# Kernel tuning notes

Hardware: AMD Instinct MI355X
Metric: run time of the kernel (lower is better)

Reference implementation:

```python
import jax, jax.numpy as jnp
import numpy as np

EPS = 1e-5


def _bn(x):
    # BatchNorm2d in training mode with gamma=1, beta=0 (as initialized in the module)
    m = x.mean(axis=(0, 2, 3), keepdims=True)
    v = jnp.mean((x - m) ** 2, axis=(0, 2, 3), keepdims=True)
    return (x - m) * jax.lax.rsqrt(v + EPS)


def _adder2d(x, w, stride, padding):
    # AdderNet pseudo-conv: out = -sum_{cin,kh,kw} |patch - w|  (negative L1 distance)
    Cout, Cin, k, _ = w.shape
    p = jax.lax.conv_general_dilated_patches(
        x, (k, k), (stride, stride), [(padding, padding), (padding, padding)]
    )  # [B, Cin*k*k, Ho, Wo], channel-major patch order matching torch unfold
    B, CKK, Ho, Wo = p.shape
    pf = p.reshape(B, CKK, Ho * Wo)          # [B, CKK, L]
    wf = w.reshape(Cout, CKK)                # [Cout, CKK]
    out = -jnp.abs(pf[:, None, :, :] - wf[None, :, :, None]).sum(axis=2)  # [B, Cout, L]
    return out.reshape(B, Cout, Ho, Wo)


def _block(x, w1, w2, stride=1, down_w=None):
    out = jax.nn.relu(_bn(_adder2d(x, w1, stride, 1)))
    out = _bn(_adder2d(out, w2, 1, 1))
    if down_w is None:
        identity = x
    else:
        identity = _bn(_adder2d(x, down_w, stride, 0))
    return jax.nn.relu(out + identity)


def setup_inputs() -> dict:
    key = jax.random.key(0)
    ks = jax.random.split(key, 10)
    f = lambda k, s: jax.random.normal(k, s, dtype=jnp.float32)
    return {
        "x": f(ks[0], (32, 3, 32, 32)),
        "conv1_w": f(ks[1], (16, 3, 3, 3)) * 0.2,
        "l1_w": f(ks[2], (6, 16, 16, 3, 3)) * 0.2,
        "l2_w0": f(ks[3], (32, 16, 3, 3)) * 0.2,
        "l2_ws": f(ks[4], (5, 32, 32, 3, 3)) * 0.2,
        "l2_down": f(ks[5], (32, 16, 1, 1)) * 0.2,
        "l3_w0": f(ks[6], (64, 32, 3, 3)) * 0.2,
        "l3_ws": f(ks[7], (5, 64, 64, 3, 3)) * 0.2,
        "l3_down": f(ks[8], (64, 32, 1, 1)) * 0.2,
        "fc_w": f(ks[9], (10, 64, 1, 1)) * 0.2,
    }


def reference(x, conv1_w, l1_w, l2_w0, l2_ws, l2_down, l3_w0, l3_ws, l3_down, fc_w):
    h = jax.lax.conv(x, conv1_w, (1, 1), 'SAME')  # ordinary conv stem
    h = jax.nn.relu(_bn(h))
    # layer1: 3 blocks, 16 channels, stride 1, no downsample
    for i in range(3):
        h = _block(h, l1_w[2 * i], l1_w[2 * i + 1], 1, None)
    # layer2: first block stride 2 with 1x1 adder downsample
    h = _block(h, l2_w0, l2_ws[0], 2, l2_down)
    h = _block(h, l2_ws[1], l2_ws[2], 1, None)
    h = _block(h, l2_ws[3], l2_ws[4], 1, None)
    # layer3
    h = _block(h, l3_w0, l3_ws[0], 2, l3_down)
    h = _block(h, l3_ws[1], l3_ws[2], 1, None)
    h = _block(h, l3_ws[3], l3_ws[4], 1, None)
    # AvgPool2d(8) on an 8x8 map == global mean
    h = h.mean(axis=(2, 3), keepdims=True)  # [B, 64, 1, 1]
    h = jnp.einsum('bchw,oc->bohw', h, fc_w[:, :, 0, 0])  # 1x1 conv classifier
    h = _bn(h)
    return h.reshape(h.shape[0], -1)  # [B, num_classes]
```

## Files before the change

### kernel.cpp

```cpp
#include <hip/hip_runtime.h>

#define BN_EPS 1e-5f

template<int C>
__device__ __forceinline__ void stats_prologue(const float2* __restrict__ part,
                                               int nPart, float invN,
                                               float2* smr, float2* pred) {
  const int TPC = 256 / C;
  int c  = threadIdx.x / TPC;
  int sl = threadIdx.x - c * TPC;
  float s = 0.f, s2 = 0.f;
  for (int j = sl; j < nPart; j += TPC) {
    float2 p = part[c * nPart + j];
    s += p.x; s2 += p.y;
  }
  pred[threadIdx.x] = make_float2(s, s2);
  __syncthreads();
  for (int st = TPC >> 1; st; st >>= 1) {
    if (sl < st) {
      pred[threadIdx.x].x += pred[threadIdx.x + st].x;
      pred[threadIdx.x].y += pred[threadIdx.x + st].y;
    }
    __syncthreads();
  }
  if (sl == 0) {
    float m   = pred[threadIdx.x].x * invN;
    float var = fmaxf(pred[threadIdx.x].y * invN - m * m, 0.f);
    smr[c] = make_float2(m, rsqrtf(var + BN_EPS));
  }
  __syncthreads();
}

template<int K, int CT, int CIN, bool INBN>
__global__ void __launch_bounds__(256)
adder_k(const float* __restrict__ x, const float2* __restrict__ inpart,
        int nPartIn, float invNIn,
        const float* __restrict__ w,
        float* __restrict__ raw, float2* __restrict__ partials,
        int B, int Cout, int H, int W, int Ho, int Wo, int stride, int pad) {
  __shared__ float2 smr[INBN ? CIN : 1];
  __shared__ float2 pred[256];
  if (INBN) stats_prologue<CIN>(inpart, nPartIn, invNIn, smr, pred);

  const int KK  = K * K;
  const int HWo = Ho * Wo;
  const int i   = blockIdx.x * 256 + threadIdx.x;
  const int b   = i / HWo;
  const int hw  = i - b * HWo;
  const int ho  = hw / Wo, wo = hw - ho * Wo;
  const int co0 = blockIdx.y * CT;

  int  off[K * K];
  bool valid[K * K];
  #pragma unroll
  for (int kh = 0; kh < K; kh++) {
    int hh = ho * stride + kh - pad;
    bool hv = (hh >= 0) & (hh < H);
    #pragma unroll
    for (int kw = 0; kw < K; kw++) {
      int ww = wo * stride + kw - pad;
      valid[kh * K + kw] = hv & (ww >= 0) & (ww < W);
      off[kh * K + kw]   = hh * W + ww;
    }
  }

  float acc[CT];
  #pragma unroll
  for (int c = 0; c < CT; c++) acc[c] = 0.f;

  const float* xb = x + (b * CIN) * H * W;
  for (int cb = 0; cb < CIN; cb += 4) {
    float p[4][K * K];
    #pragma unroll
    for (int u = 0; u < 4; u++) {
      const float* xp = xb + (cb + u) * H * W;
      float m = 0.f, r = 0.f;
      if (INBN) { float2 t = smr[cb + u]; m = t.x; r = t.y; }
      #pragma unroll
      for (int t = 0; t < KK; t++) {
        float v = valid[t] ? xp[off[t]] : 0.f;
        if (INBN) v = valid[t] ? fmaxf((v - m) * r, 0.f) : 0.f;
        p[u][t] = v;
      }
    }
    #pragma unroll
    for (int c = 0; c < CT; c++) {
      const float* wp = w + ((co0 + c) * CIN + cb) * KK;
      #pragma unroll
      for (int u = 0; u < 4; u++)
        #pragma unroll
        for (int t = 0; t < KK; t++)
          acc[c] += fabsf(p[u][t] - wp[u * KK + t]);
    }
  }

  __shared__ float2 bred[4][CT];
  float2 mine[CT];
  #pragma unroll
  for (int c = 0; c < CT; c++) {
    float v = -acc[c];
    raw[(b * Cout + co0 + c) * HWo + hw] = v;
    float sx = v, sy = v * v;
    #pragma unroll
    for (int o2 = 32; o2; o2 >>= 1) {
      sx += __shfl_down(sx, o2, 64);
      sy += __shfl_down(sy, o2, 64);
    }
    mine[c] = make_float2(sx, sy);
  }
  int lane = threadIdx.x & 63, wid = threadIdx.x >> 6;
  if (lane == 0) {
    #pragma unroll
    for (int c = 0; c < CT; c++) bred[wid][c] = mine[c];
  }
  __syncthreads();
  if (threadIdx.x < CT) {
    float2 t = bred[0][threadIdx.x];
    #pragma unroll
    for (int wv = 1; wv < 4; wv++) { t.x += bred[wv][threadIdx.x].x; t.y += bred[wv][threadIdx.x].y; }
    partials[(co0 + threadIdx.x) * gridDim.x + blockIdx.x] = t;
  }
}

__global__ void __launch_bounds__(256)
conv_stem_bn(const float* __restrict__ x, const float* __restrict__ w,
             float* __restrict__ raw, float2* __restrict__ partials) {
  const int co = blockIdx.y;
  const int i = blockIdx.x * 256 + threadIdx.x;
  const int b = i >> 10, hw = i & 1023;
  const int ho = hw >> 5, wo = hw & 31;
  float acc = 0.f;
  #pragma unroll
  for (int ci = 0; ci < 3; ci++) {
    const float* xp = x + (b * 3 + ci) * 1024;
    #pragma unroll
    for (int kh = 0; kh < 3; kh++) {
      int hh = ho + kh - 1;
      bool hv = (hh >= 0) & (hh < 32);
      #pragma unroll
      for (int kw = 0; kw < 3; kw++) {
        int ww = wo + kw - 1;
        float xv = (hv & (ww >= 0) & (ww < 32)) ? xp[hh * 32 + ww] : 0.f;
        acc += xv * w[((co * 3 + ci) * 3 + kh) * 3 + kw];
      }
    }
  }
  raw[(b * 16 + co) * 1024 + hw] = acc;

  float sx = acc, sy = acc * acc;
  #pragma unroll
  for (int o2 = 32; o2; o2 >>= 1) {
    sx += __shfl_down(sx, o2, 64);
    sy += __shfl_down(sy, o2, 64);
  }
  __shared__ float2 red[4];
  int lane = threadIdx.x & 63, wid = threadIdx.x >> 6;
  if (lane == 0) red[wid] = make_float2(sx, sy);
  __syncthreads();
  if (threadIdx.x == 0) {
    float2 t = red[0];
    t.x += red[1].x + red[2].x + red[3].x;
    t.y += red[1].y + red[2].y + red[3].y;
    partials[co * 128 + blockIdx.x] = t;
  }
}

template<int IDMODE, int C, bool POOL>
__global__ void __launch_bounds__(256)
combine_k(const float* __restrict__ raw2, const float2* __restrict__ part2, int nPart2,
          const float* __restrict__ idsrc, const float2* __restrict__ partI, int nPartI,
          float invN, float* __restrict__ out, int HW) {
  __shared__ float2 s2[C];
  __shared__ float2 sI[IDMODE ? C : 1];
  __shared__ float2 pred[256];
  stats_prologue<C>(part2, nPart2, invN, s2, pred);
  if (IDMODE) stats_prologue<C>(partI, nPartI, invN, sI, pred);

  int idx = blockIdx.x * 256 + threadIdx.x;
  int c = (idx / HW) % C;
  float2 t2 = s2[c];
  float y = (raw2[idx] - t2.x) * t2.y;
  float id;
  if (IDMODE == 0) id = idsrc[idx];
  else {
    float2 tI = sI[c];
    id = (idsrc[idx] - tI.x) * tI.y;
    if (IDMODE == 2) id = fmaxf(id, 0.f);
  }
  float h = fmaxf(y + id, 0.f);
  if (!POOL) {
    out[idx] = h;
  } else {
    float s = h;
    #pragma unroll
    for (int o2 = 32; o2; o2 >>= 1) s += __shfl_down(s, o2, 64);
    if ((threadIdx.x & 63) == 0) out[idx >> 6] = s * (1.f / 64.f);
  }
}

__global__ void head_k(const float* __restrict__ pooled, const float* __restrict__ fcw,
                       float* __restrict__ out) {
  __shared__ float logits[320];
  __shared__ float mn[10], rs[10];
  int t = threadIdx.x;
  if (t < 320) {
    int b = t / 10, o = t - b * 10;
    float s = 0.f;
    #pragma unroll
    for (int c = 0; c < 64; c++) s += pooled[b * 64 + c] * fcw[o * 64 + c];
    logits[t] = s;
  }
  __syncthreads();
  if (t < 10) {
    float s = 0.f;
    for (int b = 0; b < 32; b++) s += logits[b * 10 + t];
    float m = s * (1.f / 32.f);
    float v = 0.f;
    for (int b = 0; b < 32; b++) { float d = logits[b * 10 + t] - m; v += d * d; }
    mn[t] = m;
    rs[t] = rsqrtf(v * (1.f / 32.f) + BN_EPS);
  }
  __syncthreads();
  if (t < 320) out[t] = (logits[t] - mn[t % 10]) * rs[t % 10];
}

extern "C" void kernel_launch(void* const* d_in, const int* in_sizes, int n_in,
                              void* d_out, int out_size, void* d_ws, size_t ws_size,
                              hipStream_t stream) {
  const float* x      = (const float*)d_in[0];
  const float* conv1w = (const float*)d_in[1];
  const float* l1w    = (const float*)d_in[2];
  const float* l2w0   = (const float*)d_in[3];
  const float* l2ws   = (const float*)d_in[4];
  const float* l2down = (const float*)d_in[5];
  const float* l3w0   = (const float*)d_in[6];
  const float* l3ws   = (const float*)d_in[7];
  const float* l3down = (const float*)d_in[8];
  const float* fcw    = (const float*)d_in[9];
  float* out = (float*)d_out;

  const int T2MB = 32 * 16 * 32 * 32;
  float* base = (float*)d_ws;
  float* R0 = base + 0 * T2MB;
  float* RA = base + 1 * T2MB;
  float* RB = base + 2 * T2MB;
  float* RD = base + 3 * T2MB;
  float* H0 = base + 4 * T2MB;
  float* H1 = base + 5 * T2MB;
  float* pooled = base + 6 * T2MB;
  float2* partS = (float2*)(pooled + 4096);
  float2* partA = partS + 4096;
  float2* partB = partA + 4096;
  float2* partD = partB + 4096;

  const float inv1 = 1.f / 32768.f;
  const float inv2 = 1.f / 8192.f;
  const float inv3 = 1.f / 2048.f;

  conv_stem_bn<<<dim3(128, 16), 256, 0, stream>>>(x, conv1w, R0, partS);

  float* cur = H1;
  float* nxt = H0;

  {
    const dim3 ag(128, 8);
    adder_k<3, 2, 16, true ><<<ag, 256, 0, stream>>>(R0, partS, 128, inv1, l1w + 0 * 2304, RA, partA, 32, 16, 32, 32, 32, 32, 1, 1);
    adder_k<3, 2, 16, true ><<<ag, 256, 0, stream>>>(RA, partA, 128, inv1, l1w + 1 * 2304, RB, partB, 32, 16, 32, 32, 32, 32, 1, 1);
    combine_k<2, 16, false><<<2048, 256, 0, stream>>>(RB, partB, 128, R0, partS, 128, inv1, nxt, 1024);
    { float* t = cur; cur = nxt; nxt = t; }
    for (int i = 1; i < 3; i++) {
      adder_k<3, 2, 16, false><<<ag, 256, 0, stream>>>(cur, nullptr, 0, 0.f, l1w + (2 * i) * 2304, RA, partA, 32, 16, 32, 32, 32, 32, 1, 1);
      adder_k<3, 2, 16, true ><<<ag, 256, 0, stream>>>(RA, partA, 128, inv1, l1w + (2 * i + 1) * 2304, RB, partB, 32, 16, 32, 32, 32, 32, 1, 1);
      combine_k<0, 16, false><<<2048, 256, 0, stream>>>(RB, partB, 128, cur, nullptr, 0, inv1, nxt, 1024);
      float* t = cur; cur = nxt; nxt = t;
    }
  }

  {
    const dim3 ag(32, 16);
    adder_k<3, 2, 16, false><<<ag, 256, 0, stream>>>(cur, nullptr, 0, 0.f, l2w0, RA, partA, 32, 32, 32, 32, 16, 16, 2, 1);
    adder_k<3, 2, 32, true ><<<ag, 256, 0, stream>>>(RA, partA, 32, inv2, l2ws + 0 * 9216, RB, partB, 32, 32, 16, 16, 16, 16, 1, 1);
    adder_k<1, 2, 16, false><<<ag, 256, 0, stream>>>(cur, nullptr, 0, 0.f, l2down, RD, partD, 32, 32, 32, 32, 16, 16, 2, 0);
    combine_k<1, 32, false><<<1024, 256, 0, stream>>>(RB, partB, 32, RD, partD, 32, inv2, nxt, 256);
    { float* t = cur; cur = nxt; nxt = t; }
    for (int i = 0; i < 2; i++) {
      adder_k<3, 2, 32, false><<<ag, 256, 0, stream>>>(cur, nullptr, 0, 0.f, l2ws + (1 + 2 * i) * 9216, RA, partA, 32, 32, 16, 16, 16, 16, 1, 1);
      adder_k<3, 2, 32, true ><<<ag, 256, 0, stream>>>(RA, partA, 32, inv2, l2ws + (2 + 2 * i) * 9216, RB, partB, 32, 32, 16, 16, 16, 16, 1, 1);
      combine_k<0, 32, false><<<1024, 256, 0, stream>>>(RB, partB, 32, cur, nullptr, 0, inv2, nxt, 256);
      float* t = cur; cur = nxt; nxt = t;
    }
  }

  {
    const dim3 ag(8, 64);
    adder_k<3, 1, 32, false><<<ag, 256, 0, stream>>>(cur, nullptr, 0, 0.f, l3w0, RA, partA, 32, 64, 16, 16, 8, 8, 2, 1);
    adder_k<3, 1, 64, true ><<<ag, 256, 0, stream>>>(RA, partA, 8, inv3, l3ws + 0 * 36864, RB, partB, 32, 64, 8, 8, 8, 8, 1, 1);
    adder_k<1, 1, 32, false><<<ag, 256, 0, stream>>>(cur, nullptr, 0, 0.f, l3down, RD, partD, 32, 64, 16, 16, 8, 8, 2, 0);
    combine_k<1, 64, false><<<512, 256, 0, stream>>>(RB, partB, 8, RD, partD, 8, inv3, nxt, 64);
    { float* t = cur; cur = nxt; nxt = t; }
    adder_k<3, 1, 64, false><<<ag, 256, 0, stream>>>(cur, nullptr, 0, 0.f, l3ws + 1 * 36864, RA, partA, 32, 64, 8, 8, 8, 8, 1, 1);
    adder_k<3, 1, 64, true ><<<ag, 256, 0, stream>>>(RA, partA, 8, inv3, l3ws + 2 * 36864, RB, partB, 32, 64, 8, 8, 8, 8, 1, 1);
    combine_k<0, 64, false><<<512, 256, 0, stream>>>(RB, partB, 8, cur, nullptr, 0, inv3, nxt, 64);
    { float* t = cur; cur = nxt; nxt = t; }
    adder_k<3, 1, 64, false><<<ag, 256, 0, stream>>>(cur, nullptr, 0, 0.f, l3ws + 3 * 36864, RA, partA, 32, 64, 8, 8, 8, 8, 1, 1);
    adder_k<3, 1, 64, true ><<<ag, 256, 0, stream>>>(RA, partA, 8, inv3, l3ws + 4 * 36864, RB, partB, 32, 64, 8, 8, 8, 8, 1, 1);
    combine_k<0, 64, true ><<<512, 256, 0, stream>>>(RB, partB, 8, cur, nullptr, 0, inv3, pooled, 64);
  }

  head_k<<<1, 320, 0, stream>>>(pooled, fcw, out);
}
```

Before: 406.3 us.

## Split adder convolutions over input-channel chunks with separate reduction kernels

Replaces the per-output-channel-tile adder kernel with a split-K version: each block handles 4 output channels and 8 input channels, writing partial L1 sums to scratch planes, and a new reduce kernel sums the planes, writes raw outputs and produces BN partial statistics. The 1x1 downsample branch is fused into the strided 3x3 kernel by reusing the center tap. The goal is more parallelism and shorter per-thread loops in the small late layers, at the cost of extra kernel launches and extra global traffic for the partial planes.

```diff
diff --git a/kernel.cpp b/kernel.cpp
--- a/kernel.cpp
+++ b/kernel.cpp
@@ -31,94 +31,151 @@
   __syncthreads();
 }
 
-template<int K, int CT, int CIN, bool INBN>
-__global__ void __launch_bounds__(256)
-adder_k(const float* __restrict__ x, const float2* __restrict__ inpart,
-        int nPartIn, float invNIn,
-        const float* __restrict__ w,
-        float* __restrict__ raw, float2* __restrict__ partials,
-        int B, int Cout, int H, int W, int Ho, int Wo, int stride, int pad) {
+template<int CIN, bool INBN, bool DOWN>
+__global__ void __launch_bounds__(256, 4)
+adder_s1(const float* __restrict__ x, const float2* __restrict__ inpart,
+         int nPartIn, float invNIn,
+         const float* __restrict__ w, const float* __restrict__ wD,
+         float* __restrict__ pout, float* __restrict__ poutD,
+         int B, int Cout, int H, int W, int Ho, int Wo,
+         int stride, int pad, int plane) {
   __shared__ float2 smr[INBN ? CIN : 1];
-  __shared__ float2 pred[256];
+  __shared__ float2 pred[INBN ? 256 : 1];
   if (INBN) stats_prologue<CIN>(inpart, nPartIn, invNIn, smr, pred);
 
-  const int KK  = K * K;
   const int HWo = Ho * Wo;
   const int i   = blockIdx.x * 256 + threadIdx.x;
   const int b   = i / HWo;
   const int hw  = i - b * HWo;
   const int ho  = hw / Wo, wo = hw - ho * Wo;
-  const int co0 = blockIdx.y * CT;
-
-  int  off[K * K];
-  bool valid[K * K];
-  #pragma unroll
-  for (int kh = 0; kh < K; kh++) {
+  const int co0 = blockIdx.y * 4;
+  const int ci0 = blockIdx.z * 8;
+
+  int  off[9];
+  bool valid[9];
+  #pragma unroll
+  for (int kh = 0; kh < 3; kh++) {
     int hh = ho * stride + kh - pad;
     bool hv = (hh >= 0) & (hh < H);
     #pragma unroll
-    for (int kw = 0; kw < K; kw++) {
+    for (int kw = 0; kw < 3; kw++) {
       int ww = wo * stride + kw - pad;
-      valid[kh * K + kw] = hv & (ww >= 0) & (ww < W);
-      off[kh * K + kw]   = hh * W + ww;
-    }
-  }
-
-  float acc[CT];
-  #pragma unroll
-  for (int c = 0; c < CT; c++) acc[c] = 0.f;
-
-  const float* xb = x + (b * CIN) * H * W;
-  for (int cb = 0; cb < CIN; cb += 4) {
-    float p[4][K * K];
-    #pragma unroll
-    for (int u = 0; u < 4; u++) {
-      const float* xp = xb + (cb + u) * H * W;
-      float m = 0.f, r = 0.f;
-      if (INBN) { float2 t = smr[cb + u]; m = t.x; r = t.y; }
+      valid[kh * 3 + kw] = hv & (ww >= 0) & (ww < W);
+      off[kh * 3 + kw]   = hh * W + ww;
+    }
+  }
+
+  float p[8][9];
+  #pragma unroll
+  for (int u = 0; u < 8; u++) {
+    const float* xp = x + (b * CIN + ci0 + u) * H * W;
+    float m = 0.f, r = 0.f;
+    if (INBN) { float2 t = smr[ci0 + u]; m = t.x; r = t.y; }
+    #pragma unroll
+    for (int t = 0; t < 9; t++) {
+      float v = valid[t] ? xp[off[t]] : 0.f;
+      if (INBN) v = valid[t] ? fmaxf((v - m) * r, 0.f) : 0.f;
+      p[u][t] = v;
+    }
+  }
+
+  float acc[4];
+  float accD[DOWN ? 4 : 1];
+  #pragma unroll
+  for (int c = 0; c < 4; c++) acc[c] = 0.f;
+  if (DOWN) {
+    #pragma unroll
+    for (int c = 0; c < 4; c++) accD[c] = 0.f;
+  }
+
+  #pragma unroll
+  for (int c = 0; c < 4; c++) {
+    const float* wp = w + ((co0 + c) * CIN + ci0) * 9;
+    #pragma unroll
+    for (int u = 0; u < 8; u++)
       #pragma unroll
-      for (int t = 0; t < KK; t++) {
-        float v = valid[t] ? xp[off[t]] : 0.f;
-        if (INBN) v = valid[t] ? fmaxf((v - m) * r, 0.f) : 0.f;
-        p[u][t] = v;
-      }
-    }
-    #pragma unroll
-    for (int c = 0; c < CT; c++) {
-      const float* wp = w + ((co0 + c) * CIN + cb) * KK;
+      for (int t = 0; t < 9; t++)
+        acc[c] += fabsf(p[u][t] - wp[u * 9 + t]);
+    if (DOWN) {
+      const float* wdp = wD + (co0 + c) * CIN + ci0;
       #pragma unroll
-      for (int u = 0; u < 4; u++)
-        #pragma unroll
-        for (int t = 0; t < KK; t++)
-          acc[c] += fabsf(p[u][t] - wp[u * KK + t]);
-    }
-  }
-
-  __shared__ float2 bred[4][CT];
-  float2 mine[CT];
-  #pragma unroll
-  for (int c = 0; c < CT; c++) {
-    float v = -acc[c];
-    raw[(b * Cout + co0 + c) * HWo + hw] = v;
+      for (int u = 0; u < 8; u++)
+        accD[c] += fabsf(p[u][4] - wdp[u]);
+    }
+  }
+
+  const int zb = blockIdx.z * plane;
+  #pragma unroll
+  for (int c = 0; c < 4; c++) {
+    pout[zb + (b * Cout + co0 + c) * HWo + hw] = acc[c];
+    if (DOWN) poutD[zb + (b * Cout + co0 + c) * HWo + hw] = accD[c];
+  }
+}
+
+template<int NC, bool DUAL, bool BR>
+__global__ void __launch_bounds__(256)
+reduce_k(const float* __restrict__ pin, float* __restrict__ raw, float2* __restrict__ parts,
+         const float* __restrict__ pinD, float* __restrict__ rawD, float2* __restrict__ partsD,
+         int Cout, int HWo, int plane, int nPart) {
+  const int e = blockIdx.x * 256 + threadIdx.x;
+  const int b  = e / (Cout * HWo);
+  const int r  = e - b * Cout * HWo;
+  const int co = r / HWo;
+  const int hw = r - co * HWo;
+  const int lane = threadIdx.x & 63, wid = threadIdx.x >> 6;
+  __shared__ float2 bb[4];
+
+  {
+    float s = 0.f;
+    #pragma unroll
+    for (int z = 0; z < NC; z++) s += pin[z * plane + e];
+    float v = -s;
+    raw[e] = v;
     float sx = v, sy = v * v;
     #pragma unroll
     for (int o2 = 32; o2; o2 >>= 1) {
       sx += __shfl_down(sx, o2, 64);
       sy += __shfl_down(sy, o2, 64);
     }
-    mine[c] = make_float2(sx, sy);
-  }
-  int lane = threadIdx.x & 63, wid = threadIdx.x >> 6;
-  if (lane == 0) {
-    #pragma unroll
-    for (int c = 0; c < CT; c++) bred[wid][c] = mine[c];
-  }
-  __syncthreads();
-  if (threadIdx.x < CT) {
-    float2 t = bred[0][threadIdx.x];
-    #pragma unroll
-    for (int wv = 1; wv < 4; wv++) { t.x += bred[wv][threadIdx.x].x; t.y += bred[wv][threadIdx.x].y; }
-    partials[(co0 + threadIdx.x) * gridDim.x + blockIdx.x] = t;
+    if (BR) {
+      if (lane == 0) bb[wid] = make_float2(sx, sy);
+      __syncthreads();
+      if (threadIdx.x == 0) {
+        float2 t = bb[0];
+        t.x += bb[1].x + bb[2].x + bb[3].x;
+        t.y += bb[1].y + bb[2].y + bb[3].y;
+        parts[co * nPart + ((b * HWo + hw) >> 8)] = t;
+      }
+    } else {
+      if (lane == 0) parts[co * nPart + ((b * HWo + hw) >> 6)] = make_float2(sx, sy);
+    }
+  }
+
+  if (DUAL) {
+    if (BR) __syncthreads();
+    float s = 0.f;
+    #pragma unroll
+    for (int z = 0; z < NC; z++) s += pinD[z * plane + e];
+    float v = -s;
+    rawD[e] = v;
+    float sx = v, sy = v * v;
+    #pragma unroll
+    for (int o2 = 32; o2; o2 >>= 1) {
+      sx += __shfl_down(sx, o2, 64);
+      sy += __shfl_down(sy, o2, 64);
+    }
+    if (BR) {
+      if (lane == 0) bb[wid] = make_float2(sx, sy);
+      __syncthreads();
+      if (threadIdx.x == 0) {
+        float2 t = bb[0];
+        t.x += bb[1].x + bb[2].x + bb[3].x;
+        t.y += bb[1].y + bb[2].y + bb[3].y;
+        partsD[co * nPart + ((b * HWo + hw) >> 8)] = t;
+      }
+    } else {
+      if (lane == 0) partsD[co * nPart + ((b * HWo + hw) >> 6)] = make_float2(sx, sy);
+    }
   }
 }
 
@@ -247,64 +304,84 @@
   float* RD = base + 3 * T2MB;
   float* H0 = base + 4 * T2MB;
   float* H1 = base + 5 * T2MB;
-  float* pooled = base + 6 * T2MB;
-  float2* partS = (float2*)(pooled + 4096);
+  float* PA = base + 6 * T2MB;
+  float* PD = base + 8 * T2MB;
+  float* sm = base + 9 * T2MB;
+  float* pooled = sm;
+  float2* partS = (float2*)(sm + 4096);
   float2* partA = partS + 4096;
   float2* partB = partA + 4096;
   float2* partD = partB + 4096;
 
+  const int B = 32;
   const float inv1 = 1.f / 32768.f;
   const float inv2 = 1.f / 8192.f;
   const float inv3 = 1.f / 2048.f;
 
+  const int pl1 = 32 * 16 * 1024;
+  const int pl2 = 32 * 32 * 256;
+  const int pl3 = 32 * 64 * 64;
+
   conv_stem_bn<<<dim3(128, 16), 256, 0, stream>>>(x, conv1w, R0, partS);
 
   float* cur = H1;
   float* nxt = H0;
 
   {
-    const dim3 ag(128, 8);
-    adder_k<3, 2, 16, true ><<<ag, 256, 0, stream>>>(R0, partS, 128, inv1, l1w + 0 * 2304, RA, partA, 32, 16, 32, 32, 32, 32, 1, 1);
-    adder_k<3, 2, 16, true ><<<ag, 256, 0, stream>>>(RA, partA, 128, inv1, l1w + 1 * 2304, RB, partB, 32, 16, 32, 32, 32, 32, 1, 1);
-    combine_k<2, 16, false><<<2048, 256, 0, stream>>>(RB, partB, 128, R0, partS, 128, inv1, nxt, 1024);
-    { float* t = cur; cur = nxt; nxt = t; }
-    for (int i = 1; i < 3; i++) {
-      adder_k<3, 2, 16, false><<<ag, 256, 0, stream>>>(cur, nullptr, 0, 0.f, l1w + (2 * i) * 2304, RA, partA, 32, 16, 32, 32, 32, 32, 1, 1);
-      adder_k<3, 2, 16, true ><<<ag, 256, 0, stream>>>(RA, partA, 128, inv1, l1w + (2 * i + 1) * 2304, RB, partB, 32, 16, 32, 32, 32, 32, 1, 1);
-      combine_k<0, 16, false><<<2048, 256, 0, stream>>>(RB, partB, 128, cur, nullptr, 0, inv1, nxt, 1024);
+    const dim3 ag(128, 4, 2);
+    for (int i = 0; i < 3; i++) {
+      const float* w1 = l1w + (2 * i) * 2304;
+      const float* w2 = l1w + (2 * i + 1) * 2304;
+      if (i == 0)
+        adder_s1<16, true , false><<<ag, 256, 0, stream>>>(R0, partS, 128, inv1, w1, nullptr, PA, nullptr, B, 16, 32, 32, 32, 32, 1, 1, pl1);
+      else
+        adder_s1<16, false, false><<<ag, 256, 0, stream>>>(cur, nullptr, 0, 0.f, w1, nullptr, PA, nullptr, B, 16, 32, 32, 32, 32, 1, 1, pl1);
+      reduce_k<2, false, true><<<2048, 256, 0, stream>>>(PA, RA, partA, nullptr, nullptr, nullptr, 16, 1024, pl1, 128);
+      adder_s1<16, true , false><<<ag, 256, 0, stream>>>(RA, partA, 128, inv1, w2, nullptr, PA, nullptr, B, 16, 32, 32, 32, 32, 1, 1, pl1);
+      reduce_k<2, false, true><<<2048, 256, 0, stream>>>(PA, RB, partB, nullptr, nullptr, nullptr, 16, 1024, pl1, 128);
+      if (i == 0)
+        combine_k<2, 16, false><<<2048, 256, 0, stream>>>(RB, partB, 128, R0, partS, 128, inv1, nxt, 1024);
+      else
+        combine_k<0, 16, false><<<2048, 256, 0, stream>>>(RB, partB, 128, cur, nullptr, 0, inv1, nxt, 1024);
       float* t = cur; cur = nxt; nxt = t;
     }
   }
 
   {
-    const dim3 ag(32, 16);
-    adder_k<3, 2, 16, false><<<ag, 256, 0, stream>>>(cur, nullptr, 0, 0.f, l2w0, RA, partA, 32, 32, 32, 32, 16, 16, 2, 1);
-    adder_k<3, 2, 32, true ><<<ag, 256, 0, stream>>>(RA, partA, 32, inv2, l2ws + 0 * 9216, RB, partB, 32, 32, 16, 16, 16, 16, 1, 1);
-    adder_k<1, 2, 16, false><<<ag, 256, 0, stream>>>(cur, nullptr, 0, 0.f, l2down, RD, partD, 32, 32, 32, 32, 16, 16, 2, 0);
+    adder_s1<16, false, true ><<<dim3(32, 8, 2), 256, 0, stream>>>(cur, nullptr, 0, 0.f, l2w0, l2down, PA, PD, B, 32, 32, 32, 16, 16, 2, 1, pl2);
+    reduce_k<2, true , true><<<1024, 256, 0, stream>>>(PA, RA, partA, PD, RD, partD, 32, 256, pl2, 32);
+    adder_s1<32, true , false><<<dim3(32, 8, 4), 256, 0, stream>>>(RA, partA, 32, inv2, l2ws + 0 * 9216, nullptr, PA, nullptr, B, 32, 16, 16, 16, 16, 1, 1, pl2);
+    reduce_k<4, false, true><<<1024, 256, 0, stream>>>(PA, RB, partB, nullptr, nullptr, nullptr, 32, 256, pl2, 32);
     combine_k<1, 32, false><<<1024, 256, 0, stream>>>(RB, partB, 32, RD, partD, 32, inv2, nxt, 256);
     { float* t = cur; cur = nxt; nxt = t; }
     for (int i = 0; i < 2; i++) {
-      adder_k<3, 2, 32, false><<<ag, 256, 0, stream>>>(cur, nullptr, 0, 0.f, l2ws + (1 + 2 * i) * 9216, RA, partA, 32, 32, 16, 16, 16, 16, 1, 1);
-      adder_k<3, 2, 32, true ><<<ag, 256, 0, stream>>>(RA, partA, 32, inv2, l2ws + (2 + 2 * i) * 9216, RB, partB, 32, 32, 16, 16, 16, 16, 1, 1);
+      adder_s1<32, false, false><<<dim3(32, 8, 4), 256, 0, stream>>>(cur, nullptr, 0, 0.f, l2ws + (1 + 2 * i) * 9216, nullptr, PA, nullptr, B, 32, 16, 16, 16, 16, 1, 1, pl2);
+      reduce_k<4, false, true><<<1024, 256, 0, stream>>>(PA, RA, partA, nullptr, nullptr, nullptr, 32, 256, pl2, 32);
+      adder_s1<32, true , false><<<dim3(32, 8, 4), 256, 0, stream>>>(RA, partA, 32, inv2, l2ws + (2 + 2 * i) * 9216, nullptr, PA, nullptr, B, 32, 16, 16, 16, 16, 1, 1, pl2);
+      reduce_k<4, false, true><<<1024, 256, 0, stream>>>(PA, RB, partB, nullptr, nullptr, nullptr, 32, 256, pl2, 32);
       combine_k<0, 32, false><<<1024, 256, 0, stream>>>(RB, partB, 32, cur, nullptr, 0, inv2, nxt, 256);
       float* t = cur; cur = nxt; nxt = t;
     }
   }
 
   {
-    const dim3 ag(8, 64);
-    adder_k<3, 1, 32, false><<<ag, 256, 0, stream>>>(cur, nullptr, 0, 0.f, l3w0, RA, partA, 32, 64, 16, 16, 8, 8, 2, 1);
-    adder_k<3, 1, 64, true ><<<ag, 256, 0, stream>>>(RA, partA, 8, inv3, l3ws + 0 * 36864, RB, partB, 32, 64, 8, 8, 8, 8, 1, 1);
-    adder_k<1, 1, 32, false><<<ag, 256, 0, stream>>>(cur, nullptr, 0, 0.f, l3down, RD, partD, 32, 64, 16, 16, 8, 8, 2, 0);
-    combine_k<1, 64, false><<<512, 256, 0, stream>>>(RB, partB, 8, RD, partD, 8, inv3, nxt, 64);
+    adder_s1<32, false, true ><<<dim3(8, 16, 4), 256, 0, stream>>>(cur, nullptr, 0, 0.f, l3w0, l3down, PA, PD, B, 64, 16, 16, 8, 8, 2, 1, pl3);
+    reduce_k<4, true , false><<<512, 256, 0, stream>>>(PA, RA, partA, PD, RD, partD, 64, 64, pl3, 32);
+    adder_s1<64, true , false><<<dim3(8, 16, 8), 256, 0, stream>>>(RA, partA, 32, inv3, l3ws + 0 * 36864, nullptr, PA, nullptr, B, 64, 8, 8, 8, 8, 1, 1, pl3);
+    reduce_k<8, false, false><<<512, 256, 0, stream>>>(PA, RB, partB, nullptr, nullptr, nullptr, 64, 64, pl3, 32);
+    combine_k<1, 64, false><<<512, 256, 0, stream>>>(RB, partB, 32, RD, partD, 32, inv3, nxt, 64);
     { float* t = cur; cur = nxt; nxt = t; }
-    adder_k<3, 1, 64, false><<<ag, 256, 0, stream>>>(cur, nullptr, 0, 0.f, l3ws + 1 * 36864, RA, partA, 32, 64, 8, 8, 8, 8, 1, 1);
-    adder_k<3, 1, 64, true ><<<ag, 256, 0, stream>>>(RA, partA, 8, inv3, l3ws + 2 * 36864, RB, partB, 32, 64, 8, 8, 8, 8, 1, 1);
-    combine_k<0, 64, false><<<512, 256, 0, stream>>>(RB, partB, 8, cur, nullptr, 0, inv3, nxt, 64);
-    { float* t = cur; cur = nxt; nxt = t; }
-    adder_k<3, 1, 64, false><<<ag, 256, 0, stream>>>(cur, nullptr, 0, 0.f, l3ws + 3 * 36864, RA, partA, 32, 64, 8, 8, 8, 8, 1, 1);
-    adder_k<3, 1, 64, true ><<<ag, 256, 0, stream>>>(RA, partA, 8, inv3, l3ws + 4 * 36864, RB, partB, 32, 64, 8, 8, 8, 8, 1, 1);
-    combine_k<0, 64, true ><<<512, 256, 0, stream>>>(RB, partB, 8, cur, nullptr, 0, inv3, pooled, 64);
+    for (int i = 0; i < 2; i++) {
+      adder_s1<64, false, false><<<dim3(8, 16, 8), 256, 0, stream>>>(cur, nullptr, 0, 0.f, l3ws + (1 + 2 * i) * 36864, nullptr, PA, nullptr, B, 64, 8, 8, 8, 8, 1, 1, pl3);
+      reduce_k<8, false, false><<<512, 256, 0, stream>>>(PA, RA, partA, nullptr, nullptr, nullptr, 64, 64, pl3, 32);
+      adder_s1<64, true , false><<<dim3(8, 16, 8), 256, 0, stream>>>(RA, partA, 32, inv3, l3ws + (2 + 2 * i) * 36864, nullptr, PA, nullptr, B, 64, 8, 8, 8, 8, 1, 1, pl3);
+      reduce_k<8, false, false><<<512, 256, 0, stream>>>(PA, RB, partB, nullptr, nullptr, nullptr, 64, 64, pl3, 32);
+      if (i == 1)
+        combine_k<0, 64, true ><<<512, 256, 0, stream>>>(RB, partB, 32, cur, nullptr, 0, inv3, pooled, 64);
+      else
+        combine_k<0, 64, false><<<512, 256, 0, stream>>>(RB, partB, 32, cur, nullptr, 0, inv3, nxt, 64);
+      if (i == 0) { float* t = cur; cur = nxt; nxt = t; }
+    }
   }
 
   head_k<<<1, 320, 0, stream>>>(pooled, fcw, out);
```

Result: faster. 370.1 us (-8.9%).

## Fuse residual combine and downsample into adder kernels, split Cin across waves

Applied to the files above, without the earlier changes.

Drops the separate combine kernels by applying the previous block's BN, residual add and ReLU on the fly while loading the next adder's inputs, writing the hidden activation out as a side effect. The 1x1 downsample adder is computed inside the strided 3x3 adder using the centre tap. Each block now splits input channels across its four waves with 64 positions per block and reduces through shared memory, which gives more blocks and more parallelism. The cost is extra residual reads per input tap, plus shared-memory reduction and more template variants.

```diff
diff --git a/kernel.cpp b/kernel.cpp
--- a/kernel.cpp
+++ b/kernel.cpp
@@ -26,99 +26,130 @@
   if (sl == 0) {
     float m   = pred[threadIdx.x].x * invN;
     float var = fmaxf(pred[threadIdx.x].y * invN - m * m, 0.f);
-    smr[c] = make_float2(m, rsqrtf(var + BN_EPS));
-  }
-  __syncthreads();
-}
-
-template<int K, int CT, int CIN, bool INBN>
-__global__ void __launch_bounds__(256)
-adder_k(const float* __restrict__ x, const float2* __restrict__ inpart,
-        int nPartIn, float invNIn,
-        const float* __restrict__ w,
-        float* __restrict__ raw, float2* __restrict__ partials,
-        int B, int Cout, int H, int W, int Ho, int Wo, int stride, int pad) {
-  __shared__ float2 smr[INBN ? CIN : 1];
+    float r   = rsqrtf(var + BN_EPS);
+    smr[c] = make_float2(r, -m * r);
+  }
+  __syncthreads();
+}
+
+template<int CIN, int CT, int INM, bool DOWN, bool HWRITE>
+__global__ void __launch_bounds__(256, 4)
+adder_f(const float* __restrict__ A, const float* __restrict__ Bt,
+        const float2* __restrict__ pA, int nPA,
+        const float2* __restrict__ pB, int nPB, float invNin,
+        const float* __restrict__ w, const float* __restrict__ wD,
+        float* __restrict__ raw, float2* __restrict__ parts,
+        float* __restrict__ rawD, float2* __restrict__ partsD,
+        float* __restrict__ hout,
+        int Cout, int H, int W, int Ho, int Wo, int stride, int pad,
+        int posChunks) {
   __shared__ float2 pred[256];
-  if (INBN) stats_prologue<CIN>(inpart, nPartIn, invNIn, smr, pred);
-
-  const int KK  = K * K;
-  const int HWo = Ho * Wo;
-  const int i   = blockIdx.x * 256 + threadIdx.x;
-  const int b   = i / HWo;
-  const int hw  = i - b * HWo;
-  const int ho  = hw / Wo, wo = hw - ho * Wo;
-  const int co0 = blockIdx.y * CT;
-
-  int  off[K * K];
-  bool valid[K * K];
-  #pragma unroll
-  for (int kh = 0; kh < K; kh++) {
+  __shared__ float2 smA[(INM >= 1) ? CIN : 1];
+  __shared__ float2 smB[(INM >= 3) ? CIN : 1];
+  __shared__ float  sacc[4][CT][64];
+  __shared__ float  saccD[DOWN ? 4 : 1][DOWN ? CT : 1][DOWN ? 64 : 1];
+  if (INM >= 1) stats_prologue<CIN>(pA, nPA, invNin, smA, pred);
+  if (INM >= 3) stats_prologue<CIN>(pB, nPB, invNin, smB, pred);
+
+  const int HW = H * W, HWo = Ho * Wo;
+  const int zl = threadIdx.x >> 6, pl = threadIdx.x & 63;
+  const int pc = blockIdx.x, cog = blockIdx.y, co0 = cog * CT;
+  const int i  = pc * 64 + pl;
+  const int b  = i / HWo, hw = i - b * HWo;
+  const int ho = hw / Wo, wo = hw - ho * Wo;
+
+  int off[9]; bool val[9];
+  #pragma unroll
+  for (int kh = 0; kh < 3; kh++) {
     int hh = ho * stride + kh - pad;
     bool hv = (hh >= 0) & (hh < H);
     #pragma unroll
-    for (int kw = 0; kw < K; kw++) {
+    for (int kw = 0; kw < 3; kw++) {
       int ww = wo * stride + kw - pad;
-      valid[kh * K + kw] = hv & (ww >= 0) & (ww < W);
-      off[kh * K + kw]   = hh * W + ww;
+      val[kh * 3 + kw] = hv & (ww >= 0) & (ww < W);
+      off[kh * 3 + kw] = hh * W + ww;
     }
   }
 
   float acc[CT];
+  float accD[DOWN ? CT : 1];
   #pragma unroll
   for (int c = 0; c < CT; c++) acc[c] = 0.f;
-
-  const float* xb = x + (b * CIN) * H * W;
-  for (int cb = 0; cb < CIN; cb += 4) {
-    float p[4][K * K];
+  if (DOWN) {
+    #pragma unroll
+    for (int c = 0; c < CT; c++) accD[c] = 0.f;
+  }
+
+  const int CPZ = CIN / 4;
+  const int ci0 = zl * CPZ;
+  #pragma unroll 1
+  for (int bb = 0; bb < CPZ; bb += 4) {
+    float p[4][9];
     #pragma unroll
     for (int u = 0; u < 4; u++) {
-      const float* xp = xb + (cb + u) * H * W;
-      float m = 0.f, r = 0.f;
-      if (INBN) { float2 t = smr[cb + u]; m = t.x; r = t.y; }
+      const int ci = ci0 + bb + u;
+      const float* Ap = A + (b * CIN + ci) * HW;
+      const float* Bp = (INM >= 2) ? (Bt + (b * CIN + ci) * HW) : nullptr;
+      float2 tA = make_float2(0.f, 0.f), tB = make_float2(0.f, 0.f);
+      if (INM >= 1) tA = smA[ci];
+      if (INM >= 3) tB = smB[ci];
       #pragma unroll
-      for (int t = 0; t < KK; t++) {
-        float v = valid[t] ? xp[off[t]] : 0.f;
-        if (INBN) v = valid[t] ? fmaxf((v - m) * r, 0.f) : 0.f;
+      for (int t = 0; t < 9; t++) {
+        float v = 0.f;
+        if (val[t]) {
+          float a = Ap[off[t]];
+          if (INM == 0) v = a;
+          if (INM == 1) v = fmaxf(fmaf(a, tA.x, tA.y), 0.f);
+          if (INM == 2) v = fmaxf(fmaf(a, tA.x, tA.y) + Bp[off[t]], 0.f);
+          if (INM == 3) v = fmaxf(fmaf(a, tA.x, tA.y) + fmaf(Bp[off[t]], tB.x, tB.y), 0.f);
+          if (INM == 4) v = fmaxf(fmaf(a, tA.x, tA.y) + fmaxf(fmaf(Bp[off[t]], tB.x, tB.y), 0.f), 0.f);
+        }
         p[u][t] = v;
       }
+      if (HWRITE) {
+        if (cog == 0) hout[(b * CIN + ci) * HW + ho * W + wo] = p[u][4];
+      }
     }
     #pragma unroll
     for (int c = 0; c < CT; c++) {
-      const float* wp = w + ((co0 + c) * CIN + cb) * KK;
+      const float* wp = w + ((co0 + c) * CIN + ci0 + bb) * 9;
       #pragma unroll
       for (int u = 0; u < 4; u++)
         #pragma unroll
-        for (int t = 0; t < KK; t++)
-          acc[c] += fabsf(p[u][t] - wp[u * KK + t]);
-    }
-  }
-
-  __shared__ float2 bred[4][CT];
-  float2 mine[CT];
-  #pragma unroll
-  for (int c = 0; c < CT; c++) {
-    float v = -acc[c];
+        for (int t = 0; t < 9; t++)
+          acc[c] += fabsf(p[u][t] - wp[u * 9 + t]);
+      if (DOWN) {
+        const float* wdp = wD + (co0 + c) * CIN + ci0 + bb;
+        #pragma unroll
+        for (int u = 0; u < 4; u++) accD[c] += fabsf(p[u][4] - wdp[u]);
+      }
+    }
+  }
+
+  #pragma unroll
+  for (int c = 0; c < CT; c++) sacc[zl][c][pl] = acc[c];
+  if (DOWN) {
+    #pragma unroll
+    for (int c = 0; c < CT; c++) saccD[zl][c][pl] = accD[c];
+  }
+  __syncthreads();
+
+  if (zl < CT) {
+    const int c = zl;
+    float v = -(sacc[0][c][pl] + sacc[1][c][pl] + sacc[2][c][pl] + sacc[3][c][pl]);
     raw[(b * Cout + co0 + c) * HWo + hw] = v;
     float sx = v, sy = v * v;
     #pragma unroll
-    for (int o2 = 32; o2; o2 >>= 1) {
-      sx += __shfl_down(sx, o2, 64);
-      sy += __shfl_down(sy, o2, 64);
-    }
-    mine[c] = make_float2(sx, sy);
-  }
-  int lane = threadIdx.x & 63, wid = threadIdx.x >> 6;
-  if (lane == 0) {
-    #pragma unroll
-    for (int c = 0; c < CT; c++) bred[wid][c] = mine[c];
-  }
-  __syncthreads();
-  if (threadIdx.x < CT) {
-    float2 t = bred[0][threadIdx.x];
-    #pragma unroll
-    for (int wv = 1; wv < 4; wv++) { t.x += bred[wv][threadIdx.x].x; t.y += bred[wv][threadIdx.x].y; }
-    partials[(co0 + threadIdx.x) * gridDim.x + blockIdx.x] = t;
+    for (int o = 32; o; o >>= 1) { sx += __shfl_down(sx, o, 64); sy += __shfl_down(sy, o, 64); }
+    if (pl == 0) parts[(co0 + c) * posChunks + pc] = make_float2(sx, sy);
+    if (DOWN) {
+      float vd = -(saccD[0][c][pl] + saccD[1][c][pl] + saccD[2][c][pl] + saccD[3][c][pl]);
+      rawD[(b * Cout + co0 + c) * HWo + hw] = vd;
+      float dx = vd, dy = vd * vd;
+      #pragma unroll
+      for (int o = 32; o; o >>= 1) { dx += __shfl_down(dx, o, 64); dy += __shfl_down(dy, o, 64); }
+      if (pl == 0) partsD[(co0 + c) * posChunks + pc] = make_float2(dx, dy);
+    }
   }
 }
 
@@ -149,10 +180,7 @@
 
   float sx = acc, sy = acc * acc;
   #pragma unroll
-  for (int o2 = 32; o2; o2 >>= 1) {
-    sx += __shfl_down(sx, o2, 64);
-    sy += __shfl_down(sy, o2, 64);
-  }
+  for (int o = 32; o; o >>= 1) { sx += __shfl_down(sx, o, 64); sy += __shfl_down(sy, o, 64); }
   __shared__ float2 red[4];
   int lane = threadIdx.x & 63, wid = threadIdx.x >> 6;
   if (lane == 0) red[wid] = make_float2(sx, sy);
@@ -165,37 +193,19 @@
   }
 }
 
-template<int IDMODE, int C, bool POOL>
 __global__ void __launch_bounds__(256)
-combine_k(const float* __restrict__ raw2, const float2* __restrict__ part2, int nPart2,
-          const float* __restrict__ idsrc, const float2* __restrict__ partI, int nPartI,
-          float invN, float* __restrict__ out, int HW) {
-  __shared__ float2 s2[C];
-  __shared__ float2 sI[IDMODE ? C : 1];
+combine_pool(const float* __restrict__ raw2, const float2* __restrict__ part2, int nPart,
+             const float* __restrict__ idsrc, float invN, float* __restrict__ pooled) {
+  __shared__ float2 s2[64];
   __shared__ float2 pred[256];
-  stats_prologue<C>(part2, nPart2, invN, s2, pred);
-  if (IDMODE) stats_prologue<C>(partI, nPartI, invN, sI, pred);
-
+  stats_prologue<64>(part2, nPart, invN, s2, pred);
   int idx = blockIdx.x * 256 + threadIdx.x;
-  int c = (idx / HW) % C;
+  int c = (idx >> 6) & 63;
   float2 t2 = s2[c];
-  float y = (raw2[idx] - t2.x) * t2.y;
-  float id;
-  if (IDMODE == 0) id = idsrc[idx];
-  else {
-    float2 tI = sI[c];
-    id = (idsrc[idx] - tI.x) * tI.y;
-    if (IDMODE == 2) id = fmaxf(id, 0.f);
-  }
-  float h = fmaxf(y + id, 0.f);
-  if (!POOL) {
-    out[idx] = h;
-  } else {
-    float s = h;
-    #pragma unroll
-    for (int o2 = 32; o2; o2 >>= 1) s += __shfl_down(s, o2, 64);
-    if ((threadIdx.x & 63) == 0) out[idx >> 6] = s * (1.f / 64.f);
-  }
+  float h = fmaxf(fmaf(raw2[idx], t2.x, t2.y) + idsrc[idx], 0.f);
+  #pragma unroll
+  for (int o = 32; o; o >>= 1) h += __shfl_down(h, o, 64);
+  if ((threadIdx.x & 63) == 0) pooled[idx >> 6] = h * (1.f / 64.f);
 }
 
 __global__ void head_k(const float* __restrict__ pooled, const float* __restrict__ fcw,
@@ -239,19 +249,21 @@
   const float* fcw    = (const float*)d_in[9];
   float* out = (float*)d_out;
 
-  const int T2MB = 32 * 16 * 32 * 32;
+  const int S = 524288;
   float* base = (float*)d_ws;
-  float* R0 = base + 0 * T2MB;
-  float* RA = base + 1 * T2MB;
-  float* RB = base + 2 * T2MB;
-  float* RD = base + 3 * T2MB;
-  float* H0 = base + 4 * T2MB;
-  float* H1 = base + 5 * T2MB;
-  float* pooled = base + 6 * T2MB;
-  float2* partS = (float2*)(pooled + 4096);
-  float2* partA = partS + 4096;
-  float2* partB = partA + 4096;
-  float2* partD = partB + 4096;
+  float* R0  = base + 0 * S;
+  float* RA  = base + 1 * S;
+  float* RB0 = base + 2 * S;
+  float* RB1 = base + 3 * S;
+  float* HA  = base + 4 * S;
+  float* HB  = base + 5 * S;
+  float* RD  = base + 6 * S;
+  float* pooled = base + 7 * S;
+  float2* partS  = (float2*)(pooled + 4096);
+  float2* partA  = partS  + 8192;
+  float2* partB0 = partA  + 8192;
+  float2* partB1 = partB0 + 8192;
+  float2* partD  = partB1 + 8192;
 
   const float inv1 = 1.f / 32768.f;
   const float inv2 = 1.f / 8192.f;
@@ -259,53 +271,49 @@
 
   conv_stem_bn<<<dim3(128, 16), 256, 0, stream>>>(x, conv1w, R0, partS);
 
-  float* cur = H1;
-  float* nxt = H0;
-
-  {
-    const dim3 ag(128, 8);
-    adder_k<3, 2, 16, true ><<<ag, 256, 0, stream>>>(R0, partS, 128, inv1, l1w + 0 * 2304, RA, partA, 32, 16, 32, 32, 32, 32, 1, 1);
-    adder_k<3, 2, 16, true ><<<ag, 256, 0, stream>>>(RA, partA, 128, inv1, l1w + 1 * 2304, RB, partB, 32, 16, 32, 32, 32, 32, 1, 1);
-    combine_k<2, 16, false><<<2048, 256, 0, stream>>>(RB, partB, 128, R0, partS, 128, inv1, nxt, 1024);
-    { float* t = cur; cur = nxt; nxt = t; }
-    for (int i = 1; i < 3; i++) {
-      adder_k<3, 2, 16, false><<<ag, 256, 0, stream>>>(cur, nullptr, 0, 0.f, l1w + (2 * i) * 2304, RA, partA, 32, 16, 32, 32, 32, 32, 1, 1);
-      adder_k<3, 2, 16, true ><<<ag, 256, 0, stream>>>(RA, partA, 128, inv1, l1w + (2 * i + 1) * 2304, RB, partB, 32, 16, 32, 32, 32, 32, 1, 1);
-      combine_k<0, 16, false><<<2048, 256, 0, stream>>>(RB, partB, 128, cur, nullptr, 0, inv1, nxt, 1024);
-      float* t = cur; cur = nxt; nxt = t;
-    }
-  }
-
-  {
-    const dim3 ag(32, 16);
-    adder_k<3, 2, 16, false><<<ag, 256, 0, stream>>>(cur, nullptr, 0, 0.f, l2w0, RA, partA, 32, 32, 32, 32, 16, 16, 2, 1);
-    adder_k<3, 2, 32, true ><<<ag, 256, 0, stream>>>(RA, partA, 32, inv2, l2ws + 0 * 9216, RB, partB, 32, 32, 16, 16, 16, 16, 1, 1);
-    adder_k<1, 2, 16, false><<<ag, 256, 0, stream>>>(cur, nullptr, 0, 0.f, l2down, RD, partD, 32, 32, 32, 32, 16, 16, 2, 0);
-    combine_k<1, 32, false><<<1024, 256, 0, stream>>>(RB, partB, 32, RD, partD, 32, inv2, nxt, 256);
-    { float* t = cur; cur = nxt; nxt = t; }
-    for (int i = 0; i < 2; i++) {
-      adder_k<3, 2, 32, false><<<ag, 256, 0, stream>>>(cur, nullptr, 0, 0.f, l2ws + (1 + 2 * i) * 9216, RA, partA, 32, 32, 16, 16, 16, 16, 1, 1);
-      adder_k<3, 2, 32, true ><<<ag, 256, 0, stream>>>(RA, partA, 32, inv2, l2ws + (2 + 2 * i) * 9216, RB, partB, 32, 32, 16, 16, 16, 16, 1, 1);
-      combine_k<0, 32, false><<<1024, 256, 0, stream>>>(RB, partB, 32, cur, nullptr, 0, inv2, nxt, 256);
-      float* t = cur; cur = nxt; nxt = t;
-    }
-  }
-
-  {
-    const dim3 ag(8, 64);
-    adder_k<3, 1, 32, false><<<ag, 256, 0, stream>>>(cur, nullptr, 0, 0.f, l3w0, RA, partA, 32, 64, 16, 16, 8, 8, 2, 1);
-    adder_k<3, 1, 64, true ><<<ag, 256, 0, stream>>>(RA, partA, 8, inv3, l3ws + 0 * 36864, RB, partB, 32, 64, 8, 8, 8, 8, 1, 1);
-    adder_k<1, 1, 32, false><<<ag, 256, 0, stream>>>(cur, nullptr, 0, 0.f, l3down, RD, partD, 32, 64, 16, 16, 8, 8, 2, 0);
-    combine_k<1, 64, false><<<512, 256, 0, stream>>>(RB, partB, 8, RD, partD, 8, inv3, nxt, 64);
-    { float* t = cur; cur = nxt; nxt = t; }
-    adder_k<3, 1, 64, false><<<ag, 256, 0, stream>>>(cur, nullptr, 0, 0.f, l3ws + 1 * 36864, RA, partA, 32, 64, 8, 8, 8, 8, 1, 1);
-    adder_k<3, 1, 64, true ><<<ag, 256, 0, stream>>>(RA, partA, 8, inv3, l3ws + 2 * 36864, RB, partB, 32, 64, 8, 8, 8, 8, 1, 1);
-    combine_k<0, 64, false><<<512, 256, 0, stream>>>(RB, partB, 8, cur, nullptr, 0, inv3, nxt, 64);
-    { float* t = cur; cur = nxt; nxt = t; }
-    adder_k<3, 1, 64, false><<<ag, 256, 0, stream>>>(cur, nullptr, 0, 0.f, l3ws + 3 * 36864, RA, partA, 32, 64, 8, 8, 8, 8, 1, 1);
-    adder_k<3, 1, 64, true ><<<ag, 256, 0, stream>>>(RA, partA, 8, inv3, l3ws + 4 * 36864, RB, partB, 32, 64, 8, 8, 8, 8, 1, 1);
-    combine_k<0, 64, true ><<<512, 256, 0, stream>>>(RB, partB, 8, cur, nullptr, 0, inv3, pooled, 64);
-  }
+  const dim3 g1(512, 4);
+  adder_f<16,4,1,false,false><<<g1,256,0,stream>>>(R0, nullptr, partS, 128, nullptr, 0, inv1,
+      l1w + 0*2304, nullptr, RA, partA, nullptr, nullptr, nullptr, 16, 32,32,32,32, 1,1, 512);
+  adder_f<16,4,1,false,false><<<g1,256,0,stream>>>(RA, nullptr, partA, 512, nullptr, 0, inv1,
+      l1w + 1*2304, nullptr, RB0, partB0, nullptr, nullptr, nullptr, 16, 32,32,32,32, 1,1, 512);
+  adder_f<16,4,4,false,true ><<<g1,256,0,stream>>>(RB0, R0, partB0, 512, partS, 128, inv1,
+      l1w + 2*2304, nullptr, RA, partA, nullptr, nullptr, HA, 16, 32,32,32,32, 1,1, 512);
+  adder_f<16,4,1,false,false><<<g1,256,0,stream>>>(RA, nullptr, partA, 512, nullptr, 0, inv1,
+      l1w + 3*2304, nullptr, RB1, partB1, nullptr, nullptr, nullptr, 16, 32,32,32,32, 1,1, 512);
+  adder_f<16,4,2,false,true ><<<g1,256,0,stream>>>(RB1, HA, partB1, 512, nullptr, 0, inv1,
+      l1w + 4*2304, nullptr, RA, partA, nullptr, nullptr, HB, 16, 32,32,32,32, 1,1, 512);
+  adder_f<16,4,1,false,false><<<g1,256,0,stream>>>(RA, nullptr, partA, 512, nullptr, 0, inv1,
+      l1w + 5*2304, nullptr, RB0, partB0, nullptr, nullptr, nullptr, 16, 32,32,32,32, 1,1, 512);
+
+  const dim3 g2(128, 8);
+  adder_f<16,4,2,true ,false><<<g2,256,0,stream>>>(RB0, HB, partB0, 512, nullptr, 0, inv1,
+      l2w0, l2down, RA, partA, RD, partD, nullptr, 32, 32,32,16,16, 2,1, 128);
+  adder_f<32,4,1,false,false><<<g2,256,0,stream>>>(RA, nullptr, partA, 128, nullptr, 0, inv2,
+      l2ws + 0*9216, nullptr, RB1, partB1, nullptr, nullptr, nullptr, 32, 16,16,16,16, 1,1, 128);
+  adder_f<32,4,3,false,true ><<<g2,256,0,stream>>>(RB1, RD, partB1, 128, partD, 128, inv2,
+      l2ws + 1*9216, nullptr, RA, partA, nullptr, nullptr, HA, 32, 16,16,16,16, 1,1, 128);
+  adder_f<32,4,1,false,false><<<g2,256,0,stream>>>(RA, nullptr, partA, 128, nullptr, 0, inv2,
+      l2ws + 2*9216, nullptr, RB0, partB0, nullptr, nullptr, nullptr, 32, 16,16,16,16, 1,1, 128);
+  adder_f<32,4,2,false,true ><<<g2,256,0,stream>>>(RB0, HA, partB0, 128, nullptr, 0, inv2,
+      l2ws + 3*9216, nullptr, RA, partA, nullptr, nullptr, HB, 32, 16,16,16,16, 1,1, 128);
+  adder_f<32,4,1,false,false><<<g2,256,0,stream>>>(RA, nullptr, partA, 128, nullptr, 0, inv2,
+      l2ws + 4*9216, nullptr, RB1, partB1, nullptr, nullptr, nullptr, 32, 16,16,16,16, 1,1, 128);
+
+  const dim3 g3(32, 32);
+  adder_f<32,2,2,true ,false><<<g3,256,0,stream>>>(RB1, HB, partB1, 128, nullptr, 0, inv2,
+      l3w0, l3down, RA, partA, RD, partD, nullptr, 64, 16,16,8,8, 2,1, 32);
+  adder_f<64,2,1,false,false><<<g3,256,0,stream>>>(RA, nullptr, partA, 32, nullptr, 0, inv3,
+      l3ws + 0*36864, nullptr, RB0, partB0, nullptr, nullptr, nullptr, 64, 8,8,8,8, 1,1, 32);
+  adder_f<64,2,3,false,true ><<<g3,256,0,stream>>>(RB0, RD, partB0, 32, partD, 32, inv3,
+      l3ws + 1*36864, nullptr, RA, partA, nullptr, nullptr, HA, 64, 8,8,8,8, 1,1, 32);
+  adder_f<64,2,1,false,false><<<g3,256,0,stream>>>(RA, nullptr, partA, 32, nullptr, 0, inv3,
+      l3ws + 2*36864, nullptr, RB1, partB1, nullptr, nullptr, nullptr, 64, 8,8,8,8, 1,1, 32);
+  adder_f<64,2,2,false,true ><<<g3,256,0,stream>>>(RB1, HA, partB1, 32, nullptr, 0, inv3,
+      l3ws + 3*36864, nullptr, RA, partA, nullptr, nullptr, HB, 64, 8,8,8,8, 1,1, 32);
+  adder_f<64,2,1,false,false><<<g3,256,0,stream>>>(RA, nullptr, partA, 32, nullptr, 0, inv3,
+      l3ws + 4*36864, nullptr, RB0, partB0, nullptr, nullptr, nullptr, 64, 8,8,8,8, 1,1, 32);
+
+  combine_pool<<<512, 256, 0, stream>>>(RB0, partB0, 32, HB, inv3, pooled);
 
   head_k<<<1, 320, 0, stream>>>(pooled, fcw, out);
 }
```

New measurement: 776.9 us. 1.91x slower.
